# Kernel tuning notes

Measured on AMD Instinct MI355X. Metric: run time of the kernel, lower is better.

The kernel has to match this reference:

```python
import jax, jax.numpy as jnp
import numpy as np

B, N, H, W = 128, 16384, 512, 512  # frames, points/frame, image height/width


def setup_inputs() -> dict:
    key = jax.random.key(0)
    k1, k2 = jax.random.split(key)
    pts = jax.random.uniform(k1, (B, N, 3), dtype=jnp.float32)
    # columns: x in [0, W-1], y in [0, H-1], intensity in [0, 1]
    outputs = jnp.concatenate(
        [pts[..., 0:1] * (W - 1), pts[..., 1:2] * (H - 1), pts[..., 2:3]], axis=-1
    )
    targets = jax.random.uniform(k2, (B, H, W), dtype=jnp.float32)
    return {"outputs": outputs, "targets": targets}


def _rasterize(outputs, h, w):
    """Bilinear splat of (x, y, intensity) points into a [B, h, w] image."""
    b, n, _ = outputs.shape
    x = jnp.clip(outputs[..., 0], 0.0, w - 1)
    y = jnp.clip(outputs[..., 1], 0.0, h - 1)
    inten = outputs[..., 2]
    x0f = jnp.floor(x)
    y0f = jnp.floor(y)
    fx = x - x0f  # fractional offsets -> bilinear weights
    fy = y - y0f
    x0 = x0f.astype(jnp.int32)
    y0 = y0f.astype(jnp.int32)
    x1 = jnp.minimum(x0 + 1, w - 1)
    y1 = jnp.minimum(y0 + 1, h - 1)
    bidx = jnp.broadcast_to(jnp.arange(b, dtype=jnp.int32)[:, None], (b, n))
    img = jnp.zeros((b, h, w), dtype=outputs.dtype)
    img = img.at[bidx, y0, x0].add(inten * (1 - fx) * (1 - fy))
    img = img.at[bidx, y0, x1].add(inten * fx * (1 - fy))
    img = img.at[bidx, y1, x0].add(inten * (1 - fx) * fy)
    img = img.at[bidx, y1, x1].add(inten * fx * fy)
    return img


def reference(outputs, targets):
    h, w = targets.shape[1], targets.shape[2]
    output_image = _rasterize(outputs, h, w)
    return jnp.mean((output_image - targets) ** 2)
```

## Files before the change

### kernel.cpp

```cpp
#include <hip/hip_runtime.h>

constexpr int B = 128;
constexpr int N = 16384;
constexpr int H = 512;
constexpr int W = 512;
constexpr int HW = H * W;
constexpr long long TOT = (long long)B * HW;

constexpr int TROWS = 16;
constexpr int NTILES = H / TROWS;
constexpr int NBUCKETS = B * NTILES;
constexpr int CAP = 1024;
constexpr int NGROUPS = B * N / 4;
constexpr int BIN_BLOCKS = NGROUPS / 512;

__global__ void __launch_bounds__(512) k_bin(const float4* __restrict__ pts,
                                             float4* __restrict__ buckets,
                                             unsigned int* __restrict__ cnt) {
    __shared__ unsigned int lcnt[NTILES];
    __shared__ unsigned int lbase[NTILES];

    int tid = blockIdx.x * 512 + threadIdx.x;
    int frame = tid >> 12;
    int fb = frame * NTILES;

    if (threadIdx.x < NTILES) lcnt[threadIdx.x] = 0;
    __syncthreads();

    float4 a = pts[tid * 3 + 0];
    float4 b = pts[tid * 3 + 1];
    float4 c = pts[tid * 3 + 2];

    float xs[4] = {a.x, a.w, b.z, c.y};
    float ys[4] = {a.y, b.x, b.w, c.z};
    float is[4] = {a.z, b.y, c.x, c.w};

    int tb0[4], sl0[4], tb1[4], sl1[4];
#pragma unroll
    for (int k = 0; k < 4; ++k) {
        float x = fminf(fmaxf(xs[k], 0.0f), (float)(W - 1));
        float y = fminf(fmaxf(ys[k], 0.0f), (float)(H - 1));
        xs[k] = x; ys[k] = y;
        int y0 = (int)floorf(y);
        int y1 = min(y0 + 1, H - 1);
        int t0 = y0 >> 4;
        int t1 = y1 >> 4;
        tb0[k] = t0;
        sl0[k] = (int)atomicAdd(&lcnt[t0], 1u);
        if (t1 != t0) {
            tb1[k] = t1;
            sl1[k] = (int)atomicAdd(&lcnt[t1], 1u);
        } else {
            tb1[k] = -1; sl1[k] = 0;
        }
    }
    __syncthreads();

    if (threadIdx.x < NTILES)
        lbase[threadIdx.x] = atomicAdd(&cnt[fb + threadIdx.x], lcnt[threadIdx.x]);
    __syncthreads();

#pragma unroll
    for (int k = 0; k < 4; ++k) {
        float4 rec = make_float4(xs[k], ys[k], is[k], 0.0f);
        unsigned s0 = lbase[tb0[k]] + (unsigned)sl0[k];
        if (s0 < (unsigned)CAP)
            buckets[(size_t)(fb + tb0[k]) * CAP + s0] = rec;
        if (tb1[k] >= 0) {
            unsigned s1 = lbase[tb1[k]] + (unsigned)sl1[k];
            if (s1 < (unsigned)CAP)
                buckets[(size_t)(fb + tb1[k]) * CAP + s1] = rec;
        }
    }
}

__global__ void __launch_bounds__(512) k_tile(const float4* __restrict__ buckets,
                                              const unsigned int* __restrict__ cnt,
                                              const float* __restrict__ tgt,
                                              double* __restrict__ partials) {
    __shared__ float tile[TROWS * W];
    int bid = blockIdx.x;
    int frame = bid >> 5;
    int t = bid & (NTILES - 1);
    int r0 = t * TROWS;

    float4* t4 = (float4*)tile;
    const float4* tg = (const float4*)(tgt + (size_t)frame * HW + (size_t)r0 * W);
    for (int i = threadIdx.x; i < TROWS * W / 4; i += 512) {
        float4 v = tg[i];
        t4[i] = make_float4(-v.x, -v.y, -v.z, -v.w);
    }
    __syncthreads();

    int n = (int)min(cnt[bid], (unsigned)CAP);
    const float4* bp = buckets + (size_t)bid * CAP;
    for (int i = threadIdx.x; i < n; i += 512) {
        float4 p = bp[i];
        float x = p.x, y = p.y, inten = p.z;
        float x0f = floorf(x), y0f = floorf(y);
        float fx = x - x0f, fy = y - y0f;
        int x0 = (int)x0f, y0 = (int)y0f;
        int x1 = min(x0 + 1, W - 1);
        int y1 = min(y0 + 1, H - 1);
        int ra = y0 - r0;
        int rb = y1 - r0;
        float w00 = inten * (1.0f - fx) * (1.0f - fy);
        float w01 = inten * fx * (1.0f - fy);
        float w10 = inten * (1.0f - fx) * fy;
        float w11 = inten * fx * fy;
        if ((unsigned)ra < (unsigned)TROWS) {
            atomicAdd(&tile[ra * W + x0], w00);
            atomicAdd(&tile[ra * W + x1], w01);
        }
        if ((unsigned)rb < (unsigned)TROWS) {
            atomicAdd(&tile[rb * W + x0], w10);
            atomicAdd(&tile[rb * W + x1], w11);
        }
    }
    __syncthreads();

    double acc = 0.0;
    for (int i = threadIdx.x; i < TROWS * W / 4; i += 512) {
        float4 sv = t4[i];
        acc += (double)(sv.x * sv.x + sv.y * sv.y) + (double)(sv.z * sv.z + sv.w * sv.w);
    }

    for (int off = 32; off > 0; off >>= 1)
        acc += __shfl_down(acc, off, 64);
    __syncthreads();
    double* sacc = (double*)tile;
    int lane = threadIdx.x & 63;
    int wave = threadIdx.x >> 6;
    if (lane == 0) sacc[wave] = acc;
    __syncthreads();
    if (threadIdx.x == 0) {
        double s = 0.0;
        for (int wv = 0; wv < 8; ++wv) s += sacc[wv];
        partials[bid] = s;
    }
}

__global__ void __launch_bounds__(256) k_final(const double* __restrict__ partials,
                                               float* __restrict__ out) {
    double acc = 0.0;
    for (int i = threadIdx.x; i < NBUCKETS; i += 256)
        acc += partials[i];
    for (int off = 32; off > 0; off >>= 1)
        acc += __shfl_down(acc, off, 64);
    __shared__ double sacc[4];
    int lane = threadIdx.x & 63;
    int wave = threadIdx.x >> 6;
    if (lane == 0) sacc[wave] = acc;
    __syncthreads();
    if (threadIdx.x == 0) {
        double s = sacc[0] + sacc[1] + sacc[2] + sacc[3];
        out[0] = (float)(s / (double)TOT);
    }
}

extern "C" void kernel_launch(void* const* d_in, const int* in_sizes, int n_in,
                              void* d_out, int out_size, void* d_ws, size_t ws_size,
                              hipStream_t stream) {
    const float* pts = (const float*)d_in[0];
    const float* tgt = (const float*)d_in[1];
    float* out = (float*)d_out;

    unsigned int* cnt = (unsigned int*)d_ws;
    double* partials = (double*)((char*)d_ws + 16384);
    float4* buckets = (float4*)((char*)d_ws + 65536);

    hipMemsetAsync(cnt, 0, NBUCKETS * sizeof(unsigned int), stream);
    k_bin<<<BIN_BLOCKS, 512, 0, stream>>>((const float4*)pts, buckets, cnt);
    k_tile<<<NBUCKETS, 512, 0, stream>>>(buckets, cnt, tgt, partials);
    k_final<<<1, 256, 0, stream>>>(partials, out);
}
```

Baseline: 90.11 us.

## Expand squared error algebraically; move target sum-of-squares into binning kernel

```diff
diff --git a/kernel.cpp b/kernel.cpp
--- a/kernel.cpp
+++ b/kernel.cpp
@@ -6,6 +6,7 @@
 constexpr int W = 512;
 constexpr int HW = H * W;
 constexpr long long TOT = (long long)B * HW;
+constexpr int TOT4 = (int)(TOT / 4);
 
 constexpr int TROWS = 16;
 constexpr int NTILES = H / TROWS;
@@ -13,12 +14,21 @@
 constexpr int CAP = 1024;
 constexpr int NGROUPS = B * N / 4;
 constexpr int BIN_BLOCKS = NGROUPS / 512;
+constexpr int TPITCH = 520;
+constexpr int TILE_WORDS = TROWS * TPITCH;
+
+__device__ __forceinline__ void lds_add(float* p, float v) {
+    __hip_atomic_fetch_add(p, v, __ATOMIC_RELAXED, __HIP_MEMORY_SCOPE_WORKGROUP);
+}
 
 __global__ void __launch_bounds__(512) k_bin(const float4* __restrict__ pts,
                                              float4* __restrict__ buckets,
-                                             unsigned int* __restrict__ cnt) {
+                                             unsigned int* __restrict__ cnt,
+                                             const float4* __restrict__ tgt4,
+                                             double* __restrict__ pbin) {
     __shared__ unsigned int lcnt[NTILES];
     __shared__ unsigned int lbase[NTILES];
+    __shared__ double sacc[8];
 
     int tid = blockIdx.x * 512 + threadIdx.x;
     int frame = tid >> 12;
@@ -72,28 +82,49 @@
                 buckets[(size_t)(fb + tb1[k]) * CAP + s1] = rec;
         }
     }
+
+    double acc = 0.0;
+    for (int i = tid; i < TOT4; i += NGROUPS) {
+        float4 t = tgt4[i];
+        acc += (double)(t.x * t.x + t.y * t.y) + (double)(t.z * t.z + t.w * t.w);
+    }
+    for (int off = 32; off > 0; off >>= 1)
+        acc += __shfl_down(acc, off, 64);
+    int lane = threadIdx.x & 63;
+    int wave = threadIdx.x >> 6;
+    if (lane == 0) sacc[wave] = acc;
+    __syncthreads();
+    if (threadIdx.x == 0) {
+        double s = 0.0;
+#pragma unroll
+        for (int wv = 0; wv < 8; ++wv) s += sacc[wv];
+        pbin[blockIdx.x] = s;
+    }
 }
 
 __global__ void __launch_bounds__(512) k_tile(const float4* __restrict__ buckets,
                                               const unsigned int* __restrict__ cnt,
                                               const float* __restrict__ tgt,
-                                              double* __restrict__ partials) {
-    __shared__ float tile[TROWS * W];
+                                              double* __restrict__ ptile) {
+    __shared__ float tile[TILE_WORDS];
+    __shared__ double sacc[8];
     int bid = blockIdx.x;
     int frame = bid >> 5;
     int t = bid & (NTILES - 1);
     int r0 = t * TROWS;
 
     float4* t4 = (float4*)tile;
-    const float4* tg = (const float4*)(tgt + (size_t)frame * HW + (size_t)r0 * W);
-    for (int i = threadIdx.x; i < TROWS * W / 4; i += 512) {
-        float4 v = tg[i];
-        t4[i] = make_float4(-v.x, -v.y, -v.z, -v.w);
-    }
-    __syncthreads();
+    float4 z = make_float4(0.f, 0.f, 0.f, 0.f);
+    for (int i = threadIdx.x; i < TILE_WORDS / 4; i += 512)
+        t4[i] = z;
 
     int n = (int)min(cnt[bid], (unsigned)CAP);
+    __syncthreads();
+
     const float4* bp = buckets + (size_t)bid * CAP;
+    const float* tf = tgt + (size_t)frame * HW;
+    double c_img2 = 0.0, c_cross = 0.0;
+
     for (int i = threadIdx.x; i < n; i += 512) {
         float4 p = bp[i];
         float x = p.x, y = p.y, inten = p.z;
@@ -108,52 +139,75 @@
         float w01 = inten * fx * (1.0f - fy);
         float w10 = inten * (1.0f - fx) * fy;
         float w11 = inten * fx * fy;
-        if ((unsigned)ra < (unsigned)TROWS) {
-            atomicAdd(&tile[ra * W + x0], w00);
-            atomicAdd(&tile[ra * W + x1], w01);
-        }
-        if ((unsigned)rb < (unsigned)TROWS) {
-            atomicAdd(&tile[rb * W + x0], w10);
-            atomicAdd(&tile[rb * W + x1], w11);
-        }
-    }
-    __syncthreads();
-
-    double acc = 0.0;
-    for (int i = threadIdx.x; i < TROWS * W / 4; i += 512) {
-        float4 sv = t4[i];
-        acc += (double)(sv.x * sv.x + sv.y * sv.y) + (double)(sv.z * sv.z + sv.w * sv.w);
-    }
-
+
+        float t00 = tf[y0 * W + x0];
+        float t01 = tf[y0 * W + x1];
+        float t10 = tf[y1 * W + x0];
+        float t11 = tf[y1 * W + x1];
+
+        bool ia = (unsigned)ra < (unsigned)TROWS;
+        bool ib = (unsigned)rb < (unsigned)TROWS;
+        if (ia) {
+            lds_add(&tile[ra * TPITCH + x0], w00);
+            lds_add(&tile[ra * TPITCH + x1], w01);
+        }
+        if (ib) {
+            lds_add(&tile[rb * TPITCH + x0], w10);
+            lds_add(&tile[rb * TPITCH + x1], w11);
+        }
+        float cr = 0.0f;
+        if (ia) cr += w00 * t00 + w01 * t01;
+        if (ib) cr += w10 * t10 + w11 * t11;
+        c_cross += (double)cr;
+    }
+    __syncthreads();
+
+    {
+        int r = threadIdx.x >> 5;
+        int c0 = (threadIdx.x & 31) * 16;
+        const float4* rowp = (const float4*)&tile[r * TPITCH + c0];
+#pragma unroll
+        for (int k = 0; k < 4; ++k) {
+            float4 sv = rowp[k];
+            c_img2 += (double)(sv.x * sv.x + sv.y * sv.y) +
+                      (double)(sv.z * sv.z + sv.w * sv.w);
+        }
+    }
+
+    double acc = c_img2 - 2.0 * c_cross;
     for (int off = 32; off > 0; off >>= 1)
         acc += __shfl_down(acc, off, 64);
-    __syncthreads();
-    double* sacc = (double*)tile;
     int lane = threadIdx.x & 63;
     int wave = threadIdx.x >> 6;
     if (lane == 0) sacc[wave] = acc;
     __syncthreads();
     if (threadIdx.x == 0) {
         double s = 0.0;
+#pragma unroll
         for (int wv = 0; wv < 8; ++wv) s += sacc[wv];
-        partials[bid] = s;
-    }
-}
-
-__global__ void __launch_bounds__(256) k_final(const double* __restrict__ partials,
+        ptile[bid] = s;
+    }
+}
+
+__global__ void __launch_bounds__(512) k_final(const double* __restrict__ pbin,
+                                               const double* __restrict__ ptile,
                                                float* __restrict__ out) {
     double acc = 0.0;
-    for (int i = threadIdx.x; i < NBUCKETS; i += 256)
-        acc += partials[i];
+    for (int i = threadIdx.x; i < BIN_BLOCKS; i += 512)
+        acc += pbin[i];
+    for (int i = threadIdx.x; i < NBUCKETS; i += 512)
+        acc += ptile[i];
     for (int off = 32; off > 0; off >>= 1)
         acc += __shfl_down(acc, off, 64);
-    __shared__ double sacc[4];
+    __shared__ double sacc[8];
     int lane = threadIdx.x & 63;
     int wave = threadIdx.x >> 6;
     if (lane == 0) sacc[wave] = acc;
     __syncthreads();
     if (threadIdx.x == 0) {
-        double s = sacc[0] + sacc[1] + sacc[2] + sacc[3];
+        double s = 0.0;
+#pragma unroll
+        for (int wv = 0; wv < 8; ++wv) s += sacc[wv];
         out[0] = (float)(s / (double)TOT);
     }
 }
@@ -166,11 +220,13 @@
     float* out = (float*)d_out;
 
     unsigned int* cnt = (unsigned int*)d_ws;
-    double* partials = (double*)((char*)d_ws + 16384);
+    double* pbin  = (double*)((char*)d_ws + 16384);
+    double* ptile = (double*)((char*)d_ws + 24576);
     float4* buckets = (float4*)((char*)d_ws + 65536);
 
     hipMemsetAsync(cnt, 0, NBUCKETS * sizeof(unsigned int), stream);
-    k_bin<<<BIN_BLOCKS, 512, 0, stream>>>((const float4*)pts, buckets, cnt);
-    k_tile<<<NBUCKETS, 512, 0, stream>>>(buckets, cnt, tgt, partials);
-    k_final<<<1, 256, 0, stream>>>(partials, out);
-}
+    k_bin<<<BIN_BLOCKS, 512, 0, stream>>>((const float4*)pts, buckets, cnt,
+                                          (const float4*)tgt, pbin);
+    k_tile<<<NBUCKETS, 512, 0, stream>>>(buckets, cnt, tgt, ptile);
+    k_final<<<1, 512, 0, stream>>>(pbin, ptile, out);
+}
```

Result: slower. 104.5 us (+16.0%).

## Prefetch bucket points and targets into registers, pad LDS tile, zero-init tile

Applied to the files above, without the earlier changes.

```diff
diff --git a/kernel.cpp b/kernel.cpp
--- a/kernel.cpp
+++ b/kernel.cpp
@@ -13,6 +13,20 @@
 constexpr int CAP = 1024;
 constexpr int NGROUPS = B * N / 4;
 constexpr int BIN_BLOCKS = NGROUPS / 512;
+constexpr int TPITCH = 520;
+constexpr int TILE_WORDS = TROWS * TPITCH;
+
+__device__ __forceinline__ void lds_add(float* p, float v) {
+    __hip_atomic_fetch_add(p, v, __ATOMIC_RELAXED, __HIP_MEMORY_SCOPE_WORKGROUP);
+}
+
+__device__ __forceinline__ void pin(float4& v) {
+    asm volatile("" : "+v"(v.x), "+v"(v.y), "+v"(v.z), "+v"(v.w));
+}
+
+__global__ void __launch_bounds__(512) k_zero(unsigned int* __restrict__ cnt) {
+    cnt[blockIdx.x * 512 + threadIdx.x] = 0u;
+}
 
 __global__ void __launch_bounds__(512) k_bin(const float4* __restrict__ pts,
                                              float4* __restrict__ buckets,
@@ -74,86 +88,106 @@
     }
 }
 
+__device__ __forceinline__ void splat(float4 p, float* __restrict__ tile, int r0) {
+    float x = p.x, y = p.y, inten = p.z;
+    float x0f = floorf(x), y0f = floorf(y);
+    float fx = x - x0f, fy = y - y0f;
+    int x0 = (int)x0f, y0 = (int)y0f;
+    int x1 = min(x0 + 1, W - 1);
+    int y1 = min(y0 + 1, H - 1);
+    int ra = y0 - r0;
+    int rb = y1 - r0;
+    float w00 = inten * (1.0f - fx) * (1.0f - fy);
+    float w01 = inten * fx * (1.0f - fy);
+    float w10 = inten * (1.0f - fx) * fy;
+    float w11 = inten * fx * fy;
+    if ((unsigned)ra < (unsigned)TROWS) {
+        lds_add(&tile[ra * TPITCH + x0], w00);
+        lds_add(&tile[ra * TPITCH + x1], w01);
+    }
+    if ((unsigned)rb < (unsigned)TROWS) {
+        lds_add(&tile[rb * TPITCH + x0], w10);
+        lds_add(&tile[rb * TPITCH + x1], w11);
+    }
+}
+
 __global__ void __launch_bounds__(512) k_tile(const float4* __restrict__ buckets,
                                               const unsigned int* __restrict__ cnt,
                                               const float* __restrict__ tgt,
-                                              double* __restrict__ partials) {
-    __shared__ float tile[TROWS * W];
+                                              double* __restrict__ ptile) {
+    __shared__ __align__(16) float tile[TILE_WORDS];
+    __shared__ double sacc[8];
     int bid = blockIdx.x;
     int frame = bid >> 5;
     int t = bid & (NTILES - 1);
     int r0 = t * TROWS;
+    int tid = threadIdx.x;
+
+    const float4* bp = buckets + (size_t)bid * CAP;
+    float4 p0 = bp[tid];
+    float4 p1 = bp[tid + 512];
+    const float4* tg = (const float4*)(tgt + (size_t)frame * HW + (size_t)r0 * W);
+    float4 tv0 = tg[tid];
+    float4 tv1 = tg[tid + 512];
+    float4 tv2 = tg[tid + 1024];
+    float4 tv3 = tg[tid + 1536];
+    int n = (int)min(cnt[bid], (unsigned)CAP);
+    pin(p0); pin(p1); pin(tv0); pin(tv1); pin(tv2); pin(tv3);
 
     float4* t4 = (float4*)tile;
-    const float4* tg = (const float4*)(tgt + (size_t)frame * HW + (size_t)r0 * W);
-    for (int i = threadIdx.x; i < TROWS * W / 4; i += 512) {
-        float4 v = tg[i];
-        t4[i] = make_float4(-v.x, -v.y, -v.z, -v.w);
-    }
-    __syncthreads();
-
-    int n = (int)min(cnt[bid], (unsigned)CAP);
-    const float4* bp = buckets + (size_t)bid * CAP;
-    for (int i = threadIdx.x; i < n; i += 512) {
-        float4 p = bp[i];
-        float x = p.x, y = p.y, inten = p.z;
-        float x0f = floorf(x), y0f = floorf(y);
-        float fx = x - x0f, fy = y - y0f;
-        int x0 = (int)x0f, y0 = (int)y0f;
-        int x1 = min(x0 + 1, W - 1);
-        int y1 = min(y0 + 1, H - 1);
-        int ra = y0 - r0;
-        int rb = y1 - r0;
-        float w00 = inten * (1.0f - fx) * (1.0f - fy);
-        float w01 = inten * fx * (1.0f - fy);
-        float w10 = inten * (1.0f - fx) * fy;
-        float w11 = inten * fx * fy;
-        if ((unsigned)ra < (unsigned)TROWS) {
-            atomicAdd(&tile[ra * W + x0], w00);
-            atomicAdd(&tile[ra * W + x1], w01);
-        }
-        if ((unsigned)rb < (unsigned)TROWS) {
-            atomicAdd(&tile[rb * W + x0], w10);
-            atomicAdd(&tile[rb * W + x1], w11);
-        }
-    }
-    __syncthreads();
-
-    double acc = 0.0;
-    for (int i = threadIdx.x; i < TROWS * W / 4; i += 512) {
-        float4 sv = t4[i];
-        acc += (double)(sv.x * sv.x + sv.y * sv.y) + (double)(sv.z * sv.z + sv.w * sv.w);
-    }
-
+    float4 z = make_float4(0.f, 0.f, 0.f, 0.f);
+    for (int i = tid; i < TILE_WORDS / 4; i += 512)
+        t4[i] = z;
+    __syncthreads();
+
+    if (tid < n)       splat(p0, tile, r0);
+    if (tid + 512 < n) splat(p1, tile, r0);
+    __syncthreads();
+
+    float facc = 0.0f;
+#pragma unroll
+    for (int k = 0; k < 4; ++k) {
+        int g = tid + k * 512;
+        int r = g >> 7;
+        int c = (g & 127) << 2;
+        float4 sv = *(const float4*)&tile[r * TPITCH + c];
+        float4 tv = (k == 0) ? tv0 : (k == 1) ? tv1 : (k == 2) ? tv2 : tv3;
+        float d0 = sv.x - tv.x, d1 = sv.y - tv.y;
+        float d2 = sv.z - tv.z, d3 = sv.w - tv.w;
+        facc += d0 * d0 + d1 * d1 + d2 * d2 + d3 * d3;
+    }
+
+    double acc = (double)facc;
     for (int off = 32; off > 0; off >>= 1)
         acc += __shfl_down(acc, off, 64);
-    __syncthreads();
-    double* sacc = (double*)tile;
+    int lane = tid & 63;
+    int wave = tid >> 6;
+    if (lane == 0) sacc[wave] = acc;
+    __syncthreads();
+    if (tid == 0) {
+        double s = 0.0;
+#pragma unroll
+        for (int wv = 0; wv < 8; ++wv) s += sacc[wv];
+        ptile[bid] = s;
+    }
+}
+
+__global__ void __launch_bounds__(512) k_final(const double* __restrict__ ptile,
+                                               float* __restrict__ out) {
+    double acc = 0.0;
+    for (int i = threadIdx.x; i < NBUCKETS; i += 512)
+        acc += ptile[i];
+    for (int off = 32; off > 0; off >>= 1)
+        acc += __shfl_down(acc, off, 64);
+    __shared__ double sacc[8];
     int lane = threadIdx.x & 63;
     int wave = threadIdx.x >> 6;
     if (lane == 0) sacc[wave] = acc;
     __syncthreads();
     if (threadIdx.x == 0) {
         double s = 0.0;
+#pragma unroll
         for (int wv = 0; wv < 8; ++wv) s += sacc[wv];
-        partials[bid] = s;
-    }
-}
-
-__global__ void __launch_bounds__(256) k_final(const double* __restrict__ partials,
-                                               float* __restrict__ out) {
-    double acc = 0.0;
-    for (int i = threadIdx.x; i < NBUCKETS; i += 256)
-        acc += partials[i];
-    for (int off = 32; off > 0; off >>= 1)
-        acc += __shfl_down(acc, off, 64);
-    __shared__ double sacc[4];
-    int lane = threadIdx.x & 63;
-    int wave = threadIdx.x >> 6;
-    if (lane == 0) sacc[wave] = acc;
-    __syncthreads();
-    if (threadIdx.x == 0) {
-        double s = sacc[0] + sacc[1] + sacc[2] + sacc[3];
         out[0] = (float)(s / (double)TOT);
     }
 }
@@ -166,11 +200,11 @@
     float* out = (float*)d_out;
 
     unsigned int* cnt = (unsigned int*)d_ws;
-    double* partials = (double*)((char*)d_ws + 16384);
+    double* ptile = (double*)((char*)d_ws + 16384);
     float4* buckets = (float4*)((char*)d_ws + 65536);
 
-    hipMemsetAsync(cnt, 0, NBUCKETS * sizeof(unsigned int), stream);
+    k_zero<<<NBUCKETS / 512, 512, 0, stream>>>(cnt);
     k_bin<<<BIN_BLOCKS, 512, 0, stream>>>((const float4*)pts, buckets, cnt);
-    k_tile<<<NBUCKETS, 512, 0, stream>>>(buckets, cnt, tgt, partials);
-    k_final<<<1, 256, 0, stream>>>(partials, out);
-}
+    k_tile<<<NBUCKETS, 512, 0, stream>>>(buckets, cnt, tgt, ptile);
+    k_final<<<1, 512, 0, stream>>>(ptile, out);
+}
```

New measurement: 80.81 us. 10.3% less time.
